# Kernel tuning notes

Measured on AMD Instinct MI355X. Metric: run time of the kernel, lower is better.

## Reference

```python
import jax, jax.numpy as jnp
import numpy as np

ALPHA = 0.2        # LeakyReLU slope
N_NODES = 50000
N_REL = 500


def l2norm(x):
    n = jnp.linalg.norm(x, axis=1, keepdims=True)
    return x / jnp.maximum(n, 1e-12)


def gat_layer(x, edge, eemb, a, a2, concat):
    # x: [N, F]; edge: [2, E] (edge[0]=target, edge[1]=source); eemb: [E, R]
    dst = edge[0]
    h = jnp.concatenate([x[dst], x[edge[1]], eemb], axis=1)          # [E, 2F+R]
    m = h @ a.T                                                       # [E, out]
    p = -jax.nn.leaky_relu(m @ a2[0], ALPHA)                          # [E]
    e = jnp.exp(p)
    rowsum = jax.ops.segment_sum(e, dst, num_segments=N_NODES)       # [N]
    rowsum = jnp.where(rowsum == 0.0, 1e-12, rowsum)
    hp = jax.ops.segment_sum(e[:, None] * m, dst, num_segments=N_NODES) / rowsum[:, None]
    return jax.nn.elu(hp) if concat else hp


def setup_inputs() -> dict:
    key = jax.random.key(0)
    ks = jax.random.split(key, 12)
    E, ENH = 150000, 30000
    D, NHID, H = 200, 100, 2
    return {
        "entity_embeddings": jax.random.normal(ks[0], (N_NODES, D), jnp.float32),
        "relation_embeddings": jax.random.normal(ks[1], (N_REL, D), jnp.float32),
        "W_entities": jax.random.normal(ks[2], (D, NHID * H), jnp.float32) * 0.1,
        "W_gat": jax.random.normal(ks[3], (D, NHID * H), jnp.float32) * 0.1,
        "a_heads": jax.random.normal(ks[4], (H, NHID, 2 * D + D), jnp.float32) * 0.1,
        "a2_heads": jax.random.normal(ks[5], (H, 1, NHID), jnp.float32) * 0.1,
        "a_out": jax.random.normal(ks[6], (NHID * H, 3 * NHID * H), jnp.float32) * 0.1,
        "a2_out": jax.random.normal(ks[7], (1, NHID * H), jnp.float32) * 0.1,
        "batch_entities": jax.random.randint(ks[8], (20000,), 0, N_NODES),
        "edge_list": jax.random.randint(ks[9], (2, E), 0, N_NODES),
        "edge_type": jax.random.randint(ks[10], (E,), 0, N_REL),
        "train_indices_nhop": jax.random.randint(ks[11], (ENH, 4), 0, N_REL),
    }


def reference(entity_embeddings, relation_embeddings, W_entities, W_gat,
              a_heads, a2_heads, a_out, a2_out,
              batch_entities, edge_list, edge_type, train_indices_nhop):
    x = l2norm(entity_embeddings)
    # n-hop edges: (target, source) = (col 3, col 0); relation pair = (col 1, col 2)
    edge_nhop = jnp.stack([train_indices_nhop[:, 3], train_indices_nhop[:, 0]])
    edge_all = jnp.concatenate([edge_list, edge_nhop], axis=1)       # [2, E+Enh]
    eemb1 = jnp.concatenate([
        relation_embeddings[edge_type],
        relation_embeddings[train_indices_nhop[:, 1]] + relation_embeddings[train_indices_nhop[:, 2]],
    ], axis=0)
    # multi-head sparse attention (concat=True -> elu inside)
    heads = jax.vmap(lambda a, a2: gat_layer(x, edge_all, eemb1, a, a2, True))(a_heads, a2_heads)
    x1 = jnp.transpose(heads, (1, 0, 2)).reshape(x.shape[0], -1)     # [N, H*nhid]
    out_rel = relation_embeddings @ W_gat                             # [R, H*nhid]
    eemb2 = jnp.concatenate([
        out_rel[edge_type],
        out_rel[train_indices_nhop[:, 1]] + out_rel[train_indices_nhop[:, 2]],
    ], axis=0)
    out_ent = jax.nn.elu(gat_layer(x1, edge_all, eemb2, a_out, a2_out, False))
    mask = jnp.zeros((x.shape[0],), x.dtype).at[batch_entities].set(1.0)
    out_ent = l2norm(x @ W_entities + mask[:, None] * out_ent)
    return out_ent, out_rel, mask
```

## Files before the change

kernel.cpp:

```cpp
#include <hip/hip_runtime.h>
#include <hip/hip_bf16.h>
#include <math.h>

#define DD   200
#define NHID 100
#define OD   200
#define KP   224
#define PBS  224
#define LDSW 40

typedef __attribute__((ext_vector_type(8))) short short8;
typedef __attribute__((ext_vector_type(4))) float f32x4;

static inline int cdiv(int a, int b) { return (a + b - 1) / b; }

__device__ inline float toF(float x) { return x; }
__device__ inline float toF(__hip_bfloat16 x) { return __bfloat162float(x); }
__device__ inline void storeC(float v, float* p) { *p = v; }
__device__ inline void storeC(float v, __hip_bfloat16* p) { *p = __float2bfloat16(v); }
__device__ inline short bf16s(float f) {
    __hip_bfloat16 h = __float2bfloat16(f);
    short s; __builtin_memcpy(&s, &h, 2); return s;
}

__global__ __launch_bounds__(256)
void rownorm_inv_k(const float* __restrict__ in, float* __restrict__ sc, int M, int Dd)
{
    int wave = (blockIdx.x * blockDim.x + threadIdx.x) >> 6;
    int lane = threadIdx.x & 63;
    if (wave >= M) return;
    float ss = 0.f;
    for (int k = lane; k < Dd; k += 64) {
        float x = in[(size_t)wave * Dd + k];
        ss += x * x;
    }
    for (int o = 32; o > 0; o >>= 1) ss += __shfl_down(ss, o);
    if (lane == 0) sc[wave] = 1.f / fmaxf(sqrtf(ss), 1e-12f);
}

__global__ void prep_bt_l1(const float* __restrict__ ah, __hip_bfloat16* __restrict__ Bt)
{
    int c = blockIdx.x, k = threadIdx.x;
    if (k >= KP) return;
    int seg = c / 100, idx = c - seg * 100;
    int h = seg & 1, off = (seg >> 1) * 200;
    float v = (k < 200) ? ah[(size_t)(h * 100 + idx) * 600 + off + k] : 0.f;
    Bt[(size_t)c * KP + k] = __float2bfloat16(v);
}
__global__ void prep_bt_l2(const float* __restrict__ ao, __hip_bfloat16* __restrict__ Bt)
{
    int c = blockIdx.x, k = threadIdx.x;
    if (k >= KP) return;
    int row = (c < 200) ? c : c - 200;
    int off = (c < 200) ? 0 : 200;
    float v = (k < 200) ? ao[(size_t)row * 600 + off + k] : 0.f;
    Bt[(size_t)c * KP + k] = __float2bfloat16(v);
}
__global__ void prep_bt_fin(const float* __restrict__ W, __hip_bfloat16* __restrict__ Bt)
{
    int c = blockIdx.x, k = threadIdx.x;
    if (k >= KP) return;
    float v = (c < 200 && k < 200) ? W[(size_t)k * 200 + c] : 0.f;
    Bt[(size_t)c * KP + k] = __float2bfloat16(v);
}

__global__ __launch_bounds__(256)
void l1_both_k(const float* __restrict__ ent, const float* __restrict__ nscale,
               const __hip_bfloat16* __restrict__ Bt,
               const float* __restrict__ a2h,
               __hip_bfloat16* __restrict__ x1,
               __hip_bfloat16* __restrict__ pB,
               float* __restrict__ s1,
               int M)
{
    __shared__ __align__(16) __hip_bfloat16 Bs[400 * LDSW];
    int tid = threadIdx.x, wave = tid >> 6, lane = tid & 63;
    int quad = lane >> 4, l16 = lane & 15;
    int m0 = blockIdx.x * 64;
    int arow = m0 + wave * 16 + l16;
    bool rok = arow < M;
    float nsc = rok ? nscale[arow] : 0.f;
    const float* arp = ent + (size_t)arow * DD;

    f32x4 acc[25];
#pragma unroll
    for (int t = 0; t < 25; t++) acc[t] = (f32x4){0.f, 0.f, 0.f, 0.f};

    short8 stg[7];
#pragma unroll
    for (int i = 0; i < 7; i++) {
        int idx = tid + i * 256;
        if (idx < 1600) {
            int r = idx >> 2, c8 = idx & 3;
            stg[i] = *(const short8*)(Bt + (size_t)r * KP + c8 * 8);
        }
    }

    for (int ch = 0; ch < 7; ch++) {
#pragma unroll
        for (int i = 0; i < 7; i++) {
            int idx = tid + i * 256;
            if (idx < 1600) {
                int r = idx >> 2, c8 = idx & 3;
                *(short8*)(Bs + r * LDSW + c8 * 8) = stg[i];
            }
        }
        __syncthreads();
        if (ch < 6) {
            int kb2 = (ch + 1) * 32;
#pragma unroll
            for (int i = 0; i < 7; i++) {
                int idx = tid + i * 256;
                if (idx < 1600) {
                    int r = idx >> 2, c8 = idx & 3;
                    stg[i] = *(const short8*)(Bt + (size_t)r * KP + kb2 + c8 * 8);
                }
            }
        }
        int kb = ch * 32 + quad * 8;
        float av[8];
        if (rok && kb + 8 <= DD) {
            const float4* p = (const float4*)(arp + kb);
            float4 u0 = p[0], u1 = p[1];
            av[0] = u0.x; av[1] = u0.y; av[2] = u0.z; av[3] = u0.w;
            av[4] = u1.x; av[5] = u1.y; av[6] = u1.z; av[7] = u1.w;
        } else {
#pragma unroll
            for (int j = 0; j < 8; j++) av[j] = (rok && kb + j < DD) ? arp[kb + j] : 0.f;
        }
        short8 a;
#pragma unroll
        for (int j = 0; j < 8; j++) a[j] = bf16s(av[j] * nsc);
        const __hip_bfloat16* bp = Bs + (size_t)l16 * LDSW + quad * 8;
#pragma unroll
        for (int t = 0; t < 25; t++) {
            short8 b = *(const short8*)(bp + (size_t)t * 16 * LDSW);
            acc[t] = __builtin_amdgcn_mfma_f32_16x16x32_bf16(a, b, acc[t], 0, 0, 0);
        }
        __syncthreads();
    }

    int orow = m0 + wave * 16 + quad * 4;
    float d0[4] = {0,0,0,0}, d1[4] = {0,0,0,0}, d2[4] = {0,0,0,0}, d3[4] = {0,0,0,0};
#pragma unroll
    for (int t = 0; t < 25; t++) {
        int c = t * 16 + l16;
        int seg = c / 100, idx = c - seg * 100;
        float w = a2h[(seg & 1) * 100 + idx];
#pragma unroll
        for (int i = 0; i < 4; i++) {
            float v = acc[t][i];
            float vw = v * w;
            if (seg == 0) d0[i] += vw;
            else if (seg == 1) d1[i] += vw;
            else if (seg == 2) d2[i] += vw;
            else d3[i] += vw;
            int gm = orow + i;
            if (gm < M) {
                if (seg < 2) x1[(size_t)gm * KP + c] = __float2bfloat16(v);
                else pB[(size_t)gm * PBS + (seg - 2) * 100 + idx] = __float2bfloat16(v);
            }
        }
    }
#pragma unroll
    for (int msk = 1; msk < 16; msk <<= 1)
#pragma unroll
        for (int i = 0; i < 4; i++) {
            d0[i] += __shfl_xor(d0[i], msk);
            d1[i] += __shfl_xor(d1[i], msk);
            d2[i] += __shfl_xor(d2[i], msk);
            d3[i] += __shfl_xor(d3[i], msk);
        }
    if (l16 == 0)
#pragma unroll
        for (int i = 0; i < 4; i++) {
            int gm = orow + i;
            if (gm < M) {
                s1[gm] = d0[i]; s1[M + gm] = d1[i];
                float2 sv; sv.x = d2[i]; sv.y = d3[i];
                *(float2*)((char*)pB + (size_t)gm * (PBS * 2) + 400) = sv;
            }
        }
}

__global__ __launch_bounds__(256)
void l2_proj_k(const __hip_bfloat16* __restrict__ x1,
               const __hip_bfloat16* __restrict__ Bt,
               const float* __restrict__ a2o,
               float* __restrict__ x1A1,
               __hip_bfloat16* __restrict__ x1A2,
               float* __restrict__ s1, int M)
{
    __shared__ __align__(16) __hip_bfloat16 Bs[400 * LDSW];
    int tid = threadIdx.x, wave = tid >> 6, lane = tid & 63;
    int quad = lane >> 4, l16 = lane & 15;
    int m0 = blockIdx.x * 64;
    int arow = m0 + wave * 16 + l16;
    bool rok = arow < M;
    const __hip_bfloat16* arp = x1 + (size_t)arow * KP;

    f32x4 acc[25];
#pragma unroll
    for (int t = 0; t < 25; t++) acc[t] = (f32x4){0.f, 0.f, 0.f, 0.f};

    short8 stg[7];
#pragma unroll
    for (int i = 0; i < 7; i++) {
        int idx = tid + i * 256;
        if (idx < 1600) {
            int r = idx >> 2, c8 = idx & 3;
            stg[i] = *(const short8*)(Bt + (size_t)r * KP + c8 * 8);
        }
    }

    for (int ch = 0; ch < 7; ch++) {
#pragma unroll
        for (int i = 0; i < 7; i++) {
            int idx = tid + i * 256;
            if (idx < 1600) {
                int r = idx >> 2, c8 = idx & 3;
                *(short8*)(Bs + r * LDSW + c8 * 8) = stg[i];
            }
        }
        __syncthreads();
        if (ch < 6) {
            int kb2 = (ch + 1) * 32;
#pragma unroll
            for (int i = 0; i < 7; i++) {
                int idx = tid + i * 256;
                if (idx < 1600) {
                    int r = idx >> 2, c8 = idx & 3;
                    stg[i] = *(const short8*)(Bt + (size_t)r * KP + kb2 + c8 * 8);
                }
            }
        }
        int kb = ch * 32 + quad * 8;
        short8 a = (short8){0,0,0,0,0,0,0,0};
        if (rok) a = *(const short8*)(arp + kb);
        const __hip_bfloat16* bp = Bs + (size_t)l16 * LDSW + quad * 8;
#pragma unroll
        for (int t = 0; t < 25; t++) {
            short8 b = *(const short8*)(bp + (size_t)t * 16 * LDSW);
            acc[t] = __builtin_amdgcn_mfma_f32_16x16x32_bf16(a, b, acc[t], 0, 0, 0);
        }
        __syncthreads();
    }

    int orow = m0 + wave * 16 + quad * 4;
    float dA[4] = {0,0,0,0}, dB[4] = {0,0,0,0};
#pragma unroll
    for (int t = 0; t < 25; t++) {
        int c = t * 16 + l16;
        bool first = c < 200;
        int cc = first ? c : c - 200;
        float w = a2o[cc];
#pragma unroll
        for (int i = 0; i < 4; i++) {
            float v = acc[t][i];
            int gm = orow + i;
            if (first) {
                dA[i] += v * w;
                if (gm < M) x1A1[(size_t)gm * OD + c] = v;
            } else {
                dB[i] += v * w;
                if (gm < M) x1A2[(size_t)gm * PBS + cc] = __float2bfloat16(v);
            }
        }
    }
#pragma unroll
    for (int msk = 1; msk < 16; msk <<= 1)
#pragma unroll
        for (int i = 0; i < 4; i++) {
            dA[i] += __shfl_xor(dA[i], msk);
            dB[i] += __shfl_xor(dB[i], msk);
        }
    if (l16 == 0)
#pragma unroll
        for (int i = 0; i < 4; i++) {
            int gm = orow + i;
            if (gm < M) {
                s1[gm] = dA[i];
                *(float*)((char*)x1A2 + (size_t)gm * (PBS * 2) + 400) = dB[i];
            }
        }
}

__global__ __launch_bounds__(256)
void final_mfma_k(const float* __restrict__ ent, const float* __restrict__ nscale,
                  const __hip_bfloat16* __restrict__ Bt,
                  float* __restrict__ outent, int M)
{
    __shared__ __align__(16) __hip_bfloat16 Bs[208 * LDSW];
    int tid = threadIdx.x, wave = tid >> 6, lane = tid & 63;
    int quad = lane >> 4, l16 = lane & 15;
    int m0 = blockIdx.x * 64;
    int arow = m0 + wave * 16 + l16;
    bool rok = arow < M;
    float nsc = rok ? nscale[arow] : 0.f;
    const float* arp = ent + (size_t)arow * DD;

    f32x4 acc[13];
#pragma unroll
    for (int t = 0; t < 13; t++) acc[t] = (f32x4){0.f, 0.f, 0.f, 0.f};

    short8 stg[4];
#pragma unroll
    for (int i = 0; i < 4; i++) {
        int idx = tid + i * 256;
        if (idx < 832) {
            int r = idx >> 2, c8 = idx & 3;
            stg[i] = *(const short8*)(Bt + (size_t)r * KP + c8 * 8);
        }
    }

    for (int ch = 0; ch < 7; ch++) {
#pragma unroll
        for (int i = 0; i < 4; i++) {
            int idx = tid + i * 256;
            if (idx < 832) {
                int r = idx >> 2, c8 = idx & 3;
                *(short8*)(Bs + r * LDSW + c8 * 8) = stg[i];
            }
        }
        __syncthreads();
        if (ch < 6) {
            int kb2 = (ch + 1) * 32;
#pragma unroll
            for (int i = 0; i < 4; i++) {
                int idx = tid + i * 256;
                if (idx < 832) {
                    int r = idx >> 2, c8 = idx & 3;
                    stg[i] = *(const short8*)(Bt + (size_t)r * KP + kb2 + c8 * 8);
                }
            }
        }
        int kb = ch * 32 + quad * 8;
        float av[8];
        if (rok && kb + 8 <= DD) {
            const float4* p = (const float4*)(arp + kb);
            float4 u0 = p[0], u1 = p[1];
            av[0] = u0.x; av[1] = u0.y; av[2] = u0.z; av[3] = u0.w;
            av[4] = u1.x; av[5] = u1.y; av[6] = u1.z; av[7] = u1.w;
        } else {
#pragma unroll
            for (int j = 0; j < 8; j++) av[j] = (rok && kb + j < DD) ? arp[kb + j] : 0.f;
        }
        short8 a;
#pragma unroll
        for (int j = 0; j < 8; j++) a[j] = bf16s(av[j] * nsc);
        const __hip_bfloat16* bp = Bs + (size_t)l16 * LDSW + quad * 8;
#pragma unroll
        for (int t = 0; t < 13; t++) {
            short8 b = *(const short8*)(bp + (size_t)t * 16 * LDSW);
            acc[t] = __builtin_amdgcn_mfma_f32_16x16x32_bf16(a, b, acc[t], 0, 0, 0);
        }
        __syncthreads();
    }

    int orow = m0 + wave * 16 + quad * 4;
    float ss[4] = {0.f, 0.f, 0.f, 0.f};
#pragma unroll
    for (int t = 0; t < 13; t++) {
        int gn = t * 16 + l16;
#pragma unroll
        for (int i = 0; i < 4; i++) {
            int gm = orow + i;
            float v = 0.f;
            if (gn < OD && gm < M) v = acc[t][i] + outent[(size_t)gm * OD + gn];
            acc[t][i] = v;
            ss[i] += v * v;
        }
    }
#pragma unroll
    for (int msk = 1; msk < 16; msk <<= 1)
#pragma unroll
        for (int i = 0; i < 4; i++) ss[i] += __shfl_xor(ss[i], msk);
    float scl[4];
#pragma unroll
    for (int i = 0; i < 4; i++) scl[i] = 1.f / fmaxf(sqrtf(ss[i]), 1e-12f);
#pragma unroll
    for (int t = 0; t < 13; t++) {
        int gn = t * 16 + l16;
        if (gn >= OD) continue;
#pragma unroll
        for (int i = 0; i < 4; i++) {
            int gm = orow + i;
            if (gm < M) outent[(size_t)gm * OD + gn] = acc[t][i] * scl[i];
        }
    }
}

#define KPAD 48
template<bool BTr, typename AT, typename CT>
__global__ __launch_bounds__(256)
void gemm_mfma_k(const AT* __restrict__ A, int lda, const float* __restrict__ ascale,
                 const float* __restrict__ B, int ldb, int colOff,
                 CT* __restrict__ C, int ldc, int M, int Nc, int K)
{
    __shared__ __align__(16) __hip_bfloat16 As[64][KPAD];
    __shared__ __align__(16) __hip_bfloat16 Bs[64][KPAD];
    int tid  = threadIdx.x;
    int wave = tid >> 6, lane = tid & 63;
    int quad = lane >> 4, l16 = lane & 15;
    int n0 = blockIdx.x * 64, m0 = blockIdx.y * 64;
    f32x4 acc[4];
#pragma unroll
    for (int t = 0; t < 4; t++) acc[t] = (f32x4){0.f, 0.f, 0.f, 0.f};

    for (int k0 = 0; k0 < K; k0 += 32) {
        {
            int m = tid >> 2, kc = (tid & 3) * 8;
            int gm = m0 + m;
            float scale = (ascale && gm < M) ? ascale[gm] : 1.f;
#pragma unroll
            for (int j = 0; j < 8; j++) {
                int gk = k0 + kc + j;
                float v = 0.f;
                if (gm < M && gk < K) v = toF(A[(size_t)gm * lda + gk]) * scale;
                As[m][kc + j] = __float2bfloat16(v);
            }
        }
        if (BTr) {
            int n = tid >> 2, kc = (tid & 3) * 8;
            int gn = n0 + n;
#pragma unroll
            for (int j = 0; j < 8; j++) {
                int gk = k0 + kc + j;
                float v = 0.f;
                if (gn < Nc && gk < K) v = B[(size_t)gn * ldb + colOff + gk];
                Bs[n][kc + j] = __float2bfloat16(v);
            }
        } else {
            int n = tid & 63, kq = tid >> 6;
            int gn = n0 + n;
#pragma unroll
            for (int j = 0; j < 8; j++) {
                int gk = k0 + kq * 8 + j;
                float v = 0.f;
                if (gn < Nc && gk < K) v = B[(size_t)gk * ldb + gn];
                Bs[n][kq * 8 + j] = __float2bfloat16(v);
            }
        }
        __syncthreads();
        short8 a = *(const short8*)&As[wave * 16 + l16][quad * 8];
#pragma unroll
        for (int t = 0; t < 4; t++) {
            short8 b = *(const short8*)&Bs[t * 16 + l16][quad * 8];
            acc[t] = __builtin_amdgcn_mfma_f32_16x16x32_bf16(a, b, acc[t], 0, 0, 0);
        }
        __syncthreads();
    }
#pragma unroll
    for (int t = 0; t < 4; t++) {
        int gn = n0 + t * 16 + l16;
        if (gn >= Nc) continue;
#pragma unroll
        for (int i = 0; i < 4; i++) {
            int gm = m0 + wave * 16 + quad * 4 + i;
            if (gm < M) storeC(acc[t][i], &C[(size_t)gm * ldc + gn]);
        }
    }
}

template<typename T>
__global__ __launch_bounds__(256)
void rowdot_k(const T* __restrict__ mat, int ld, int coff,
              const float* __restrict__ vec,
              float* __restrict__ outp, int M, int Dd)
{
    int wave = (blockIdx.x * blockDim.x + threadIdx.x) >> 6;
    int lane = threadIdx.x & 63;
    if (wave >= M) return;
    float s = 0.f;
    for (int k = lane; k < Dd; k += 64)
        s += toF(mat[(size_t)wave * ld + coff + k]) * vec[k];
    for (int o = 32; o > 0; o >>= 1) s += __shfl_down(s, o);
    if (lane == 0) outp[wave] = s;
}

__device__ inline void decode_edge(const int* __restrict__ el, int E,
                                   const int* __restrict__ etype,
                                   const int* __restrict__ tin, int e,
                                   int& dst, int& src, int& r1, int& r2)
{
    if (e < E) { dst = el[e]; src = el[E + e]; r1 = etype[e]; r2 = -1; }
    else {
        int j = e - E;
        dst = tin[j * 4 + 3]; src = tin[j * 4 + 0];
        r1 = tin[j * 4 + 1];  r2 = tin[j * 4 + 2];
    }
}

__global__ void hist_k(const int* __restrict__ el, int E, const int* __restrict__ etype,
                       const int* __restrict__ tin, int Etot, int* __restrict__ cnt)
{
    int e = blockIdx.x * blockDim.x + threadIdx.x;
    if (e >= Etot) return;
    int dst, src, r1, r2; decode_edge(el, E, etype, tin, e, dst, src, r1, r2);
    atomicAdd(&cnt[dst], 1);
}

__global__ __launch_bounds__(1024)
void scan1_k(const int* __restrict__ cnt, int* __restrict__ start,
             int* __restrict__ aux, int n)
{
    __shared__ int tmp[1024];
    int i = blockIdx.x * 1024 + threadIdx.x;
    int v = (i < n) ? cnt[i] : 0;
    tmp[threadIdx.x] = v;
    __syncthreads();
    for (int o = 1; o < 1024; o <<= 1) {
        int t = (threadIdx.x >= (unsigned)o) ? tmp[threadIdx.x - o] : 0;
        __syncthreads();
        tmp[threadIdx.x] += t;
        __syncthreads();
    }
    if (i < n) start[i] = tmp[threadIdx.x] - v;
    if (threadIdx.x == 1023) aux[blockIdx.x] = tmp[1023];
}

__global__ void scan2_k(int* __restrict__ aux, int nb)
{
    if (threadIdx.x == 0 && blockIdx.x == 0) {
        int s = 0;
        for (int i = 0; i < nb; i++) { int v = aux[i]; aux[i] = s; s += v; }
    }
}

__global__ __launch_bounds__(1024)
void scan3_k(int* __restrict__ start, const int* __restrict__ aux, int n, int Etot)
{
    int i = blockIdx.x * 1024 + threadIdx.x;
    if (i < n) start[i] += aux[blockIdx.x];
    if (i == 0) start[n] = Etot;
}

__global__ void fill_k(const int* __restrict__ el, int E, const int* __restrict__ etype,
                       const int* __restrict__ tin, int Etot,
                       const int* __restrict__ start, int* __restrict__ fill,
                       int2* __restrict__ csr)
{
    int e = blockIdx.x * blockDim.x + threadIdx.x;
    if (e >= Etot) return;
    int dst, src, r1, r2; decode_edge(el, E, etype, tin, e, dst, src, r1, r2);
    int p = start[dst] + atomicAdd(&fill[dst], 1);
    unsigned r2s = (r2 >= 0) ? (unsigned)r2 : 0xFFFFu;
    csr[p] = make_int2(src, (int)((r2s << 16) | (unsigned)r1));
}

__global__ __launch_bounds__(256)
void gather_l1_k(const int* __restrict__ start, const int2* __restrict__ csr,
                 const float* __restrict__ s1,
                 const float* __restrict__ srel2, int R_,
                 const __hip_bfloat16* __restrict__ pB,
                 const float* __restrict__ rpf2,
                 __hip_bfloat16* __restrict__ x1, int N)
{
    int n = (blockIdx.x * blockDim.x + threadIdx.x) >> 6;
    int lane = threadIdx.x & 63;
    if (n >= N) return;
    int b0 = start[n], b1 = start[n + 1];
    float s1h0 = s1[n], s1h1 = s1[N + n];
    float rs0 = 0.f, rs1 = 0.f;
    float a00 = 0.f, a01 = 0.f, a10 = 0.f, a11 = 0.f;
    int k0 = lane, k1 = lane + 64;
    bool k1ok = k1 < 100;
    const float* rph1 = rpf2 + (size_t)R_ * 100;

    int idx = b0;
    for (; idx + 1 < b1; idx += 2) {
        int2 eA = csr[idx], eB = csr[idx + 1];
        unsigned eyA = (unsigned)eA.y, eyB = (unsigned)eB.y;
        int r1A = (int)(eyA & 0xFFFFu), r1B = (int)(eyB & 0xFFFFu);
        unsigned r2A = eyA >> 16, r2B = eyB >> 16;
        const __hip_bfloat16* rA = pB + (size_t)eA.x * PBS;
        const __hip_bfloat16* rB = pB + (size_t)eB.x * PBS;
        float2 sA = *(const float2*)(rA + 200);
        float2 sB = *(const float2*)(rB + 200);
        float vA00 = toF(rA[k0]), vA10 = toF(rA[100 + k0]);
        float vB00 = toF(rB[k0]), vB10 = toF(rB[100 + k0]);
        float vA01 = 0.f, vA11 = 0.f, vB01 = 0.f, vB11 = 0.f;
        if (k1ok) {
            vA01 = toF(rA[k1]); vA11 = toF(rA[100 + k1]);
            vB01 = toF(rB[k1]); vB11 = toF(rB[100 + k1]);
        }
        const float* qA0 = rpf2 + (size_t)r1A * 100;
        const float* qA1 = rph1 + (size_t)r1A * 100;
        const float* qB0 = rpf2 + (size_t)r1B * 100;
        const float* qB1 = rph1 + (size_t)r1B * 100;
        float srA0 = srel2[r1A], srA1 = srel2[R_ + r1A];
        float srB0 = srel2[r1B], srB1 = srel2[R_ + r1B];
        vA00 += qA0[k0]; vA10 += qA1[k0];
        vB00 += qB0[k0]; vB10 += qB1[k0];
        if (k1ok) {
            vA01 += qA0[k1]; vA11 += qA1[k1];
            vB01 += qB0[k1]; vB11 += qB1[k1];
        }
        if (r2A != 0xFFFFu) {
            const float* t0 = rpf2 + (size_t)r2A * 100;
            const float* t1 = rph1 + (size_t)r2A * 100;
            srA0 += srel2[(int)r2A]; srA1 += srel2[R_ + (int)r2A];
            vA00 += t0[k0]; vA10 += t1[k0];
            if (k1ok) { vA01 += t0[k1]; vA11 += t1[k1]; }
        }
        if (r2B != 0xFFFFu) {
            const float* t0 = rpf2 + (size_t)r2B * 100;
            const float* t1 = rph1 + (size_t)r2B * 100;
            srB0 += srel2[(int)r2B]; srB1 += srel2[R_ + (int)r2B];
            vB00 += t0[k0]; vB10 += t1[k0];
            if (k1ok) { vB01 += t0[k1]; vB11 += t1[k1]; }
        }
        float zA0 = s1h0 + sA.x + srA0, zA1 = s1h1 + sA.y + srA1;
        float zB0 = s1h0 + sB.x + srB0, zB1 = s1h1 + sB.y + srB1;
        float wA0 = expf(-(zA0 > 0.f ? zA0 : 0.2f * zA0));
        float wA1 = expf(-(zA1 > 0.f ? zA1 : 0.2f * zA1));
        float wB0 = expf(-(zB0 > 0.f ? zB0 : 0.2f * zB0));
        float wB1 = expf(-(zB1 > 0.f ? zB1 : 0.2f * zB1));
        rs0 += wA0 + wB0; rs1 += wA1 + wB1;
        a00 += wA0 * vA00 + wB0 * vB00;
        a01 += wA0 * vA01 + wB0 * vB01;
        a10 += wA1 * vA10 + wB1 * vB10;
        a11 += wA1 * vA11 + wB1 * vB11;
    }
    if (idx < b1) {
        int2 eg = csr[idx];
        unsigned ey = (unsigned)eg.y;
        int r1 = (int)(ey & 0xFFFFu);
        unsigned r2 = ey >> 16;
        const __hip_bfloat16* rA = pB + (size_t)eg.x * PBS;
        float2 sA = *(const float2*)(rA + 200);
        float v00 = toF(rA[k0]), v10 = toF(rA[100 + k0]);
        float v01 = 0.f, v11 = 0.f;
        if (k1ok) { v01 = toF(rA[k1]); v11 = toF(rA[100 + k1]); }
        const float* q0 = rpf2 + (size_t)r1 * 100;
        const float* q1 = rph1 + (size_t)r1 * 100;
        float sr0 = srel2[r1], sr1 = srel2[R_ + r1];
        v00 += q0[k0]; v10 += q1[k0];
        if (k1ok) { v01 += q0[k1]; v11 += q1[k1]; }
        if (r2 != 0xFFFFu) {
            const float* t0 = rpf2 + (size_t)r2 * 100;
            const float* t1 = rph1 + (size_t)r2 * 100;
            sr0 += srel2[(int)r2]; sr1 += srel2[R_ + (int)r2];
            v00 += t0[k0]; v10 += t1[k0];
            if (k1ok) { v01 += t0[k1]; v11 += t1[k1]; }
        }
        float z0 = s1h0 + sA.x + sr0, z1 = s1h1 + sA.y + sr1;
        float w0 = expf(-(z0 > 0.f ? z0 : 0.2f * z0));
        float w1 = expf(-(z1 > 0.f ? z1 : 0.2f * z1));
        rs0 += w0; rs1 += w1;
        a00 += w0 * v00; a01 += w0 * v01;
        a10 += w1 * v10; a11 += w1 * v11;
    }

    float i0 = rs0 > 0.f ? 1.f / rs0 : 0.f;
    float i1 = rs1 > 0.f ? 1.f / rs1 : 0.f;
    __hip_bfloat16* xr = x1 + (size_t)n * KP;
    float hp;
    hp = rs0 > 0.f ? toF(xr[k0]) + a00 * i0 : 0.f;
    xr[k0] = __float2bfloat16(hp > 0.f ? hp : expf(hp) - 1.f);
    hp = rs1 > 0.f ? toF(xr[100 + k0]) + a10 * i1 : 0.f;
    xr[100 + k0] = __float2bfloat16(hp > 0.f ? hp : expf(hp) - 1.f);
    if (k1ok) {
        hp = rs0 > 0.f ? toF(xr[k1]) + a01 * i0 : 0.f;
        xr[k1] = __float2bfloat16(hp > 0.f ? hp : expf(hp) - 1.f);
        hp = rs1 > 0.f ? toF(xr[100 + k1]) + a11 * i1 : 0.f;
        xr[100 + k1] = __float2bfloat16(hp > 0.f ? hp : expf(hp) - 1.f);
    }
}

__global__ __launch_bounds__(256)
void gather_l2_k(const int* __restrict__ start, const int2* __restrict__ csr,
                 const float* __restrict__ s1,
                 const float* __restrict__ srel,
                 const __hip_bfloat16* __restrict__ x1A2,
                 const float* __restrict__ rpf,
                 const float* __restrict__ maskf,
                 float* __restrict__ outent, int N)
{
    int n = (blockIdx.x * blockDim.x + threadIdx.x) >> 6;
    int lane = threadIdx.x & 63;
    if (n >= N) return;
    int b0 = start[n], b1 = start[n + 1];
    float s1n = s1[n];
    float rs = 0.f;
    float a[4] = {0.f, 0.f, 0.f, 0.f};

    int idx = b0;
    for (; idx + 1 < b1; idx += 2) {
        int2 eA = csr[idx], eB = csr[idx + 1];
        unsigned eyA = (unsigned)eA.y, eyB = (unsigned)eB.y;
        int r1A = (int)(eyA & 0xFFFFu), r1B = (int)(eyB & 0xFFFFu);
        unsigned r2A = eyA >> 16, r2B = eyB >> 16;
        const __hip_bfloat16* xA = x1A2 + (size_t)eA.x * PBS;
        const __hip_bfloat16* xB = x1A2 + (size_t)eB.x * PBS;
        float s2A = *(const float*)(xA + 200);
        float s2B = *(const float*)(xB + 200);
        float srA = srel[r1A] + (r2A != 0xFFFFu ? srel[(int)r2A] : 0.f);
        float srB = srel[r1B] + (r2B != 0xFFFFu ? srel[(int)r2B] : 0.f);
        const float* qA1 = rpf + (size_t)r1A * 200;
        const float* qB1 = rpf + (size_t)r1B * 200;
        const float* qA2 = (r2A != 0xFFFFu) ? (rpf + (size_t)r2A * 200) : nullptr;
        const float* qB2 = (r2B != 0xFFFFu) ? (rpf + (size_t)r2B * 200) : nullptr;
        float zA = s1n + s2A + srA, zB = s1n + s2B + srB;
        float wA = expf(-(zA > 0.f ? zA : 0.2f * zA));
        float wB = expf(-(zB > 0.f ? zB : 0.2f * zB));
        rs += wA + wB;
#pragma unroll
        for (int s = 0; s < 4; s++) {
            int k = lane + 64 * s;
            if (k < 200) {
                float vA = toF(xA[k]) + qA1[k] + (qA2 ? qA2[k] : 0.f);
                float vB = toF(xB[k]) + qB1[k] + (qB2 ? qB2[k] : 0.f);
                a[s] += wA * vA + wB * vB;
            }
        }
    }
    if (idx < b1) {
        int2 eg = csr[idx];
        unsigned ey = (unsigned)eg.y;
        int r1 = (int)(ey & 0xFFFFu);
        unsigned r2 = ey >> 16;
        const __hip_bfloat16* xs = x1A2 + (size_t)eg.x * PBS;
        float s2v = *(const float*)(xs + 200);
        float sr = srel[r1] + (r2 != 0xFFFFu ? srel[(int)r2] : 0.f);
        float z = s1n + s2v + sr;
        float w = expf(-(z > 0.f ? z : 0.2f * z));
        rs += w;
        const float* q1 = rpf + (size_t)r1 * 200;
        const float* q2 = (r2 != 0xFFFFu) ? (rpf + (size_t)r2 * 200) : nullptr;
#pragma unroll
        for (int s = 0; s < 4; s++) {
            int k = lane + 64 * s;
            if (k < 200) {
                float v = toF(xs[k]) + q1[k] + (q2 ? q2[k] : 0.f);
                a[s] += w * v;
            }
        }
    }

    float inv = rs > 0.f ? 1.f / rs : 0.f;
    float mk = maskf[n];
    float* orow = outent + (size_t)n * 200;
#pragma unroll
    for (int s = 0; s < 4; s++) {
        int k = lane + 64 * s;
        if (k < 200) {
            float hp = rs > 0.f ? orow[k] + a[s] * inv : 0.f;
            float e = hp > 0.f ? hp : expf(hp) - 1.f;
            orow[k] = mk * e;
        }
    }
}

__global__ void scatter_mask_k(const int* __restrict__ batch, int NB,
                               float* __restrict__ masko)
{
    int i = blockIdx.x * blockDim.x + threadIdx.x;
    if (i >= NB) return;
    masko[batch[i]] = 1.0f;
}

extern "C" void kernel_launch(void* const* d_in, const int* in_sizes, int n_in,
                              void* d_out, int out_size, void* d_ws, size_t ws_size,
                              hipStream_t stream)
{
    const float* ent      = (const float*)d_in[0];
    const float* rel      = (const float*)d_in[1];
    const float* W_ent    = (const float*)d_in[2];
    const float* W_gat    = (const float*)d_in[3];
    const float* a_heads  = (const float*)d_in[4];
    const float* a2_heads = (const float*)d_in[5];
    const float* a_out    = (const float*)d_in[6];
    const float* a2_out   = (const float*)d_in[7];
    const int* batch = (const int*)d_in[8];
    const int* el    = (const int*)d_in[9];
    const int* etype = (const int*)d_in[10];
    const int* tin   = (const int*)d_in[11];

    const int N   = in_sizes[0] / DD;
    const int R   = in_sizes[1] / DD;
    const int NB  = in_sizes[8];
    const int E   = in_sizes[9] / 2;
    const int ENH = in_sizes[11] / 4;
    const int Etot = E + ENH;

    char* ws = (char*)d_ws;
    size_t off = 0;
    auto take = [&](size_t bytes) { size_t o = off; off += (bytes + 255) & ~(size_t)255; return o; };
    size_t o_R1   = take((size_t)N * KP * 2);
    size_t o_R2   = take((size_t)N * PBS * 2);
    size_t o_rpf  = take((size_t)2 * R * 100 * 4);
    size_t o_bt1  = take((size_t)400 * KP * 2);
    size_t o_bt2  = take((size_t)400 * KP * 2);
    size_t o_btf  = take((size_t)208 * KP * 2);
    size_t o_nsc  = take((size_t)N * 4);
    size_t o_s1   = take((size_t)2 * N * 4);
    size_t o_srel = take((size_t)2 * R * 4);
    size_t o_csr  = take((size_t)Etot * 8);
    size_t o_str  = take((size_t)(N + 1) * 4);
    size_t o_aux  = take((size_t)64 * 4);

    __hip_bfloat16* x1   = (__hip_bfloat16*)(ws + o_R1);
    __hip_bfloat16* pB   = (__hip_bfloat16*)(ws + o_R2);
    __hip_bfloat16* x1A2 = (__hip_bfloat16*)(ws + o_R2);
    float* rpf2   = (float*)(ws + o_rpf);
    __hip_bfloat16* bt1 = (__hip_bfloat16*)(ws + o_bt1);
    __hip_bfloat16* bt2 = (__hip_bfloat16*)(ws + o_bt2);
    __hip_bfloat16* btf = (__hip_bfloat16*)(ws + o_btf);
    float* nscale = (float*)(ws + o_nsc);
    float* s1     = (float*)(ws + o_s1);
    float* srel2  = (float*)(ws + o_srel);
    int2*  csr    = (int2*)(ws + o_csr);
    int*   cnt    = (int*)(ws + o_s1);
    int*   startA = (int*)(ws + o_str);
    int*   aux    = (int*)(ws + o_aux);

    float* out       = (float*)d_out;
    float* out_ent   = out;
    float* out_rel_o = out + (size_t)N * OD;
    float* out_mask  = out + (size_t)N * OD + (size_t)R * OD;

    const int nblk = cdiv(N, 64);
    const int nbScan = cdiv(N, 1024);

    rownorm_inv_k<<<cdiv(N, 4), 256, 0, stream>>>(ent, nscale, N, DD);
    prep_bt_l1<<<400, 256, 0, stream>>>(a_heads, bt1);
    prep_bt_l2<<<400, 256, 0, stream>>>(a_out, bt2);
    prep_bt_fin<<<208, 256, 0, stream>>>(W_ent, btf);
    hipMemsetAsync(x1, 0, (size_t)N * KP * 2, stream);
    gemm_mfma_k<false, float, float><<<dim3(cdiv(OD, 64), cdiv(R, 64)), 256, 0, stream>>>(
        rel, DD, nullptr, W_gat, OD, 0, out_rel_o, OD, R, OD, DD);

    hipMemsetAsync(cnt, 0, (size_t)N * 4, stream);
    hist_k<<<cdiv(Etot, 256), 256, 0, stream>>>(el, E, etype, tin, Etot, cnt);
    scan1_k<<<nbScan, 1024, 0, stream>>>(cnt, startA, aux, N);
    scan2_k<<<1, 64, 0, stream>>>(aux, nbScan);
    scan3_k<<<nbScan, 1024, 0, stream>>>(startA, aux, N, Etot);
    hipMemsetAsync(cnt, 0, (size_t)N * 4, stream);
    fill_k<<<cdiv(Etot, 256), 256, 0, stream>>>(el, E, etype, tin, Etot, startA, cnt, csr);

    l1_both_k<<<nblk, 256, 0, stream>>>(ent, nscale, bt1, a2_heads, x1, pB, s1, N);
    for (int h = 0; h < 2; h++) {
        const float* ah  = a_heads + (size_t)h * NHID * 600;
        const float* a2h = a2_heads + (size_t)h * NHID;
        gemm_mfma_k<true, float, float><<<dim3(cdiv(NHID, 64), cdiv(R, 64)), 256, 0, stream>>>(
            rel, DD, nullptr, ah, 600, 400, rpf2 + (size_t)h * R * NHID, NHID, R, NHID, DD);
        rowdot_k<float><<<cdiv(R, 4), 256, 0, stream>>>(
            rpf2 + (size_t)h * R * NHID, NHID, 0, a2h, srel2 + (size_t)h * R, R, NHID);
    }
    gather_l1_k<<<cdiv(N, 4), 256, 0, stream>>>(
        startA, csr, s1, srel2, R, pB, rpf2, x1, N);

    l2_proj_k<<<nblk, 256, 0, stream>>>(x1, bt2, a2_out, out_ent, x1A2, s1, N);
    gemm_mfma_k<true, float, float><<<dim3(cdiv(OD, 64), cdiv(R, 64)), 256, 0, stream>>>(
        out_rel_o, OD, nullptr, a_out, 600, 400, rpf2, OD, R, OD, OD);
    rowdot_k<float><<<cdiv(R, 4), 256, 0, stream>>>(rpf2, OD, 0, a2_out, srel2, R, OD);

    hipMemsetAsync(out_mask, 0, (size_t)N * 4, stream);
    scatter_mask_k<<<cdiv(NB, 256), 256, 0, stream>>>(batch, NB, out_mask);
    gather_l2_k<<<cdiv(N, 4), 256, 0, stream>>>(
        startA, csr, s1, srel2, x1A2, rpf2, out_mask, out_ent, N);

    final_mfma_k<<<nblk, 256, 0, stream>>>(ent, nscale, btf, out_ent, N);
}
```

Measured before the change: 521.3 us.

## Interleave head data and unroll edge gathers by four with packed loads

The per-source projection buffer pB and the relation projection/score buffers now store the two heads interleaved, so gather_l1 reads both heads with a single 32-bit or float2 load. Both gather kernels are rewritten to process four edges per iteration without branches, masking invalid edges and absent second relations with zero weights. The layer-2 gather also uses paired bf16/float2 loads and stores. This is meant to raise memory-level parallelism and cut load instruction count in the latency-bound CSR gathers, at the cost of more registers and some wasted loads on padded edges.

```diff
diff --git a/kernel.cpp b/kernel.cpp
--- a/kernel.cpp
+++ b/kernel.cpp
@@ -22,6 +22,8 @@
     __hip_bfloat16 h = __float2bfloat16(f);
     short s; __builtin_memcpy(&s, &h, 2); return s;
 }
+__device__ inline float bfLo(unsigned u) { return __uint_as_float(u << 16); }
+__device__ inline float bfHi(unsigned u) { return __uint_as_float(u & 0xFFFF0000u); }
 
 __global__ __launch_bounds__(256)
 void rownorm_inv_k(const float* __restrict__ in, float* __restrict__ sc, int M, int Dd)
@@ -158,7 +160,7 @@
             int gm = orow + i;
             if (gm < M) {
                 if (seg < 2) x1[(size_t)gm * KP + c] = __float2bfloat16(v);
-                else pB[(size_t)gm * PBS + (seg - 2) * 100 + idx] = __float2bfloat16(v);
+                else pB[(size_t)gm * PBS + idx * 2 + (seg - 2)] = __float2bfloat16(v);
             }
         }
     }
@@ -395,7 +397,8 @@
 __global__ __launch_bounds__(256)
 void gemm_mfma_k(const AT* __restrict__ A, int lda, const float* __restrict__ ascale,
                  const float* __restrict__ B, int ldb, int colOff,
-                 CT* __restrict__ C, int ldc, int M, int Nc, int K)
+                 CT* __restrict__ C, int ldc, int cs, int co,
+                 int M, int Nc, int K)
 {
     __shared__ __align__(16) __hip_bfloat16 As[64][KPAD];
     __shared__ __align__(16) __hip_bfloat16 Bs[64][KPAD];
@@ -457,25 +460,25 @@
 #pragma unroll
         for (int i = 0; i < 4; i++) {
             int gm = m0 + wave * 16 + quad * 4 + i;
-            if (gm < M) storeC(acc[t][i], &C[(size_t)gm * ldc + gn]);
+            if (gm < M) storeC(acc[t][i], &C[(size_t)gm * ldc + (size_t)gn * cs + co]);
         }
     }
 }
 
 template<typename T>
 __global__ __launch_bounds__(256)
-void rowdot_k(const T* __restrict__ mat, int ld, int coff,
+void rowdot_k(const T* __restrict__ mat, int ld, int coff, int ks,
               const float* __restrict__ vec,
-              float* __restrict__ outp, int M, int Dd)
+              float* __restrict__ outp, int os, int oo, int M, int Dd)
 {
     int wave = (blockIdx.x * blockDim.x + threadIdx.x) >> 6;
     int lane = threadIdx.x & 63;
     if (wave >= M) return;
     float s = 0.f;
     for (int k = lane; k < Dd; k += 64)
-        s += toF(mat[(size_t)wave * ld + coff + k]) * vec[k];
+        s += toF(mat[(size_t)wave * ld + coff + (size_t)k * ks]) * vec[k];
     for (int o = 32; o > 0; o >>= 1) s += __shfl_down(s, o);
-    if (lane == 0) outp[wave] = s;
+    if (lane == 0) outp[wave * os + oo] = s;
 }
 
 __device__ inline void decode_edge(const int* __restrict__ el, int E,
@@ -551,7 +554,7 @@
 __global__ __launch_bounds__(256)
 void gather_l1_k(const int* __restrict__ start, const int2* __restrict__ csr,
                  const float* __restrict__ s1,
-                 const float* __restrict__ srel2, int R_,
+                 const float* __restrict__ srel2,
                  const __hip_bfloat16* __restrict__ pB,
                  const float* __restrict__ rpf2,
                  __hip_bfloat16* __restrict__ x1, int N)
@@ -562,108 +565,67 @@
     int b0 = start[n], b1 = start[n + 1];
     float s1h0 = s1[n], s1h1 = s1[N + n];
     float rs0 = 0.f, rs1 = 0.f;
-    float a00 = 0.f, a01 = 0.f, a10 = 0.f, a11 = 0.f;
+    float2 acc0 = {0.f, 0.f};
+    float2 acc1 = {0.f, 0.f};
     int k0 = lane, k1 = lane + 64;
     bool k1ok = k1 < 100;
-    const float* rph1 = rpf2 + (size_t)R_ * 100;
-
-    int idx = b0;
-    for (; idx + 1 < b1; idx += 2) {
-        int2 eA = csr[idx], eB = csr[idx + 1];
-        unsigned eyA = (unsigned)eA.y, eyB = (unsigned)eB.y;
-        int r1A = (int)(eyA & 0xFFFFu), r1B = (int)(eyB & 0xFFFFu);
-        unsigned r2A = eyA >> 16, r2B = eyB >> 16;
-        const __hip_bfloat16* rA = pB + (size_t)eA.x * PBS;
-        const __hip_bfloat16* rB = pB + (size_t)eB.x * PBS;
-        float2 sA = *(const float2*)(rA + 200);
-        float2 sB = *(const float2*)(rB + 200);
-        float vA00 = toF(rA[k0]), vA10 = toF(rA[100 + k0]);
-        float vB00 = toF(rB[k0]), vB10 = toF(rB[100 + k0]);
-        float vA01 = 0.f, vA11 = 0.f, vB01 = 0.f, vB11 = 0.f;
-        if (k1ok) {
-            vA01 = toF(rA[k1]); vA11 = toF(rA[100 + k1]);
-            vB01 = toF(rB[k1]); vB11 = toF(rB[100 + k1]);
-        }
-        const float* qA0 = rpf2 + (size_t)r1A * 100;
-        const float* qA1 = rph1 + (size_t)r1A * 100;
-        const float* qB0 = rpf2 + (size_t)r1B * 100;
-        const float* qB1 = rph1 + (size_t)r1B * 100;
-        float srA0 = srel2[r1A], srA1 = srel2[R_ + r1A];
-        float srB0 = srel2[r1B], srB1 = srel2[R_ + r1B];
-        vA00 += qA0[k0]; vA10 += qA1[k0];
-        vB00 += qB0[k0]; vB10 += qB1[k0];
-        if (k1ok) {
-            vA01 += qA0[k1]; vA11 += qA1[k1];
-            vB01 += qB0[k1]; vB11 += qB1[k1];
-        }
-        if (r2A != 0xFFFFu) {
-            const float* t0 = rpf2 + (size_t)r2A * 100;
-            const float* t1 = rph1 + (size_t)r2A * 100;
-            srA0 += srel2[(int)r2A]; srA1 += srel2[R_ + (int)r2A];
-            vA00 += t0[k0]; vA10 += t1[k0];
-            if (k1ok) { vA01 += t0[k1]; vA11 += t1[k1]; }
-        }
-        if (r2B != 0xFFFFu) {
-            const float* t0 = rpf2 + (size_t)r2B * 100;
-            const float* t1 = rph1 + (size_t)r2B * 100;
-            srB0 += srel2[(int)r2B]; srB1 += srel2[R_ + (int)r2B];
-            vB00 += t0[k0]; vB10 += t1[k0];
-            if (k1ok) { vB01 += t0[k1]; vB11 += t1[k1]; }
-        }
-        float zA0 = s1h0 + sA.x + srA0, zA1 = s1h1 + sA.y + srA1;
-        float zB0 = s1h0 + sB.x + srB0, zB1 = s1h1 + sB.y + srB1;
-        float wA0 = expf(-(zA0 > 0.f ? zA0 : 0.2f * zA0));
-        float wA1 = expf(-(zA1 > 0.f ? zA1 : 0.2f * zA1));
-        float wB0 = expf(-(zB0 > 0.f ? zB0 : 0.2f * zB0));
-        float wB1 = expf(-(zB1 > 0.f ? zB1 : 0.2f * zB1));
-        rs0 += wA0 + wB0; rs1 += wA1 + wB1;
-        a00 += wA0 * vA00 + wB0 * vB00;
-        a01 += wA0 * vA01 + wB0 * vB01;
-        a10 += wA1 * vA10 + wB1 * vB10;
-        a11 += wA1 * vA11 + wB1 * vB11;
-    }
-    if (idx < b1) {
-        int2 eg = csr[idx];
-        unsigned ey = (unsigned)eg.y;
-        int r1 = (int)(ey & 0xFFFFu);
-        unsigned r2 = ey >> 16;
-        const __hip_bfloat16* rA = pB + (size_t)eg.x * PBS;
-        float2 sA = *(const float2*)(rA + 200);
-        float v00 = toF(rA[k0]), v10 = toF(rA[100 + k0]);
-        float v01 = 0.f, v11 = 0.f;
-        if (k1ok) { v01 = toF(rA[k1]); v11 = toF(rA[100 + k1]); }
-        const float* q0 = rpf2 + (size_t)r1 * 100;
-        const float* q1 = rph1 + (size_t)r1 * 100;
-        float sr0 = srel2[r1], sr1 = srel2[R_ + r1];
-        v00 += q0[k0]; v10 += q1[k0];
-        if (k1ok) { v01 += q0[k1]; v11 += q1[k1]; }
-        if (r2 != 0xFFFFu) {
-            const float* t0 = rpf2 + (size_t)r2 * 100;
-            const float* t1 = rph1 + (size_t)r2 * 100;
-            sr0 += srel2[(int)r2]; sr1 += srel2[R_ + (int)r2];
-            v00 += t0[k0]; v10 += t1[k0];
-            if (k1ok) { v01 += t0[k1]; v11 += t1[k1]; }
-        }
-        float z0 = s1h0 + sA.x + sr0, z1 = s1h1 + sA.y + sr1;
-        float w0 = expf(-(z0 > 0.f ? z0 : 0.2f * z0));
-        float w1 = expf(-(z1 > 0.f ? z1 : 0.2f * z1));
-        rs0 += w0; rs1 += w1;
-        a00 += w0 * v00; a01 += w0 * v01;
-        a10 += w1 * v10; a11 += w1 * v11;
+    int k1c = k1ok ? k1 : 0;
+
+    for (int base = b0; base < b1; base += 4) {
+        float2 vk0[4], vk1[4];
+        float w0[4], w1[4];
+#pragma unroll
+        for (int u = 0; u < 4; u++) {
+            int id = base + u;
+            bool val = id < b1;
+            int2 eg = csr[val ? id : b0];
+            unsigned ey = (unsigned)eg.y;
+            int r1 = (int)(ey & 0xFFFFu);
+            unsigned r2u = ey >> 16;
+            bool has2 = (r2u != 0xFFFFu);
+            int r2 = has2 ? (int)r2u : 0;
+            float f2 = has2 ? 1.f : 0.f;
+            const __hip_bfloat16* rA = pB + (unsigned)((unsigned)eg.x * PBS);
+            float2 sA = *(const float2*)(rA + 200);
+            unsigned pw0 = *(const unsigned*)(rA + 2 * k0);
+            unsigned pw1 = *(const unsigned*)(rA + 2 * k1c);
+            const float2* q1 = (const float2*)(rpf2 + (unsigned)r1 * 200);
+            const float2* q2 = (const float2*)(rpf2 + (unsigned)r2 * 200);
+            float2 sr1v = *(const float2*)(srel2 + r1 * 2);
+            float2 sr2v = *(const float2*)(srel2 + r2 * 2);
+            float2 q1a = q1[k0], q1b = q1[k1c];
+            float2 q2a = q2[k0], q2b = q2[k1c];
+            vk0[u].x = bfLo(pw0) + q1a.x + f2 * q2a.x;
+            vk0[u].y = bfHi(pw0) + q1a.y + f2 * q2a.y;
+            vk1[u].x = bfLo(pw1) + q1b.x + f2 * q2b.x;
+            vk1[u].y = bfHi(pw1) + q1b.y + f2 * q2b.y;
+            float z0 = s1h0 + sA.x + sr1v.x + f2 * sr2v.x;
+            float z1 = s1h1 + sA.y + sr1v.y + f2 * sr2v.y;
+            float e0 = expf(-(z0 > 0.f ? z0 : 0.2f * z0));
+            float e1 = expf(-(z1 > 0.f ? z1 : 0.2f * z1));
+            w0[u] = val ? e0 : 0.f;
+            w1[u] = val ? e1 : 0.f;
+        }
+#pragma unroll
+        for (int u = 0; u < 4; u++) {
+            rs0 += w0[u]; rs1 += w1[u];
+            acc0.x += w0[u] * vk0[u].x; acc0.y += w1[u] * vk0[u].y;
+            acc1.x += w0[u] * vk1[u].x; acc1.y += w1[u] * vk1[u].y;
+        }
     }
 
     float i0 = rs0 > 0.f ? 1.f / rs0 : 0.f;
     float i1 = rs1 > 0.f ? 1.f / rs1 : 0.f;
     __hip_bfloat16* xr = x1 + (size_t)n * KP;
     float hp;
-    hp = rs0 > 0.f ? toF(xr[k0]) + a00 * i0 : 0.f;
+    hp = rs0 > 0.f ? toF(xr[k0]) + acc0.x * i0 : 0.f;
     xr[k0] = __float2bfloat16(hp > 0.f ? hp : expf(hp) - 1.f);
-    hp = rs1 > 0.f ? toF(xr[100 + k0]) + a10 * i1 : 0.f;
+    hp = rs1 > 0.f ? toF(xr[100 + k0]) + acc0.y * i1 : 0.f;
     xr[100 + k0] = __float2bfloat16(hp > 0.f ? hp : expf(hp) - 1.f);
     if (k1ok) {
-        hp = rs0 > 0.f ? toF(xr[k1]) + a01 * i0 : 0.f;
+        hp = rs0 > 0.f ? toF(xr[k1]) + acc1.x * i0 : 0.f;
         xr[k1] = __float2bfloat16(hp > 0.f ? hp : expf(hp) - 1.f);
-        hp = rs1 > 0.f ? toF(xr[100 + k1]) + a11 * i1 : 0.f;
+        hp = rs1 > 0.f ? toF(xr[100 + k1]) + acc1.y * i1 : 0.f;
         xr[100 + k1] = __float2bfloat16(hp > 0.f ? hp : expf(hp) - 1.f);
     }
 }
@@ -683,72 +645,73 @@
     int b0 = start[n], b1 = start[n + 1];
     float s1n = s1[n];
     float rs = 0.f;
-    float a[4] = {0.f, 0.f, 0.f, 0.f};
-
-    int idx = b0;
-    for (; idx + 1 < b1; idx += 2) {
-        int2 eA = csr[idx], eB = csr[idx + 1];
-        unsigned eyA = (unsigned)eA.y, eyB = (unsigned)eB.y;
-        int r1A = (int)(eyA & 0xFFFFu), r1B = (int)(eyB & 0xFFFFu);
-        unsigned r2A = eyA >> 16, r2B = eyB >> 16;
-        const __hip_bfloat16* xA = x1A2 + (size_t)eA.x * PBS;
-        const __hip_bfloat16* xB = x1A2 + (size_t)eB.x * PBS;
-        float s2A = *(const float*)(xA + 200);
-        float s2B = *(const float*)(xB + 200);
-        float srA = srel[r1A] + (r2A != 0xFFFFu ? srel[(int)r2A] : 0.f);
-        float srB = srel[r1B] + (r2B != 0xFFFFu ? srel[(int)r2B] : 0.f);
-        const float* qA1 = rpf + (size_t)r1A * 200;
-        const float* qB1 = rpf + (size_t)r1B * 200;
-        const float* qA2 = (r2A != 0xFFFFu) ? (rpf + (size_t)r2A * 200) : nullptr;
-        const float* qB2 = (r2B != 0xFFFFu) ? (rpf + (size_t)r2B * 200) : nullptr;
-        float zA = s1n + s2A + srA, zB = s1n + s2B + srB;
-        float wA = expf(-(zA > 0.f ? zA : 0.2f * zA));
-        float wB = expf(-(zB > 0.f ? zB : 0.2f * zB));
-        rs += wA + wB;
-#pragma unroll
-        for (int s = 0; s < 4; s++) {
-            int k = lane + 64 * s;
-            if (k < 200) {
-                float vA = toF(xA[k]) + qA1[k] + (qA2 ? qA2[k] : 0.f);
-                float vB = toF(xB[k]) + qB1[k] + (qB2 ? qB2[k] : 0.f);
-                a[s] += wA * vA + wB * vB;
-            }
-        }
-    }
-    if (idx < b1) {
-        int2 eg = csr[idx];
-        unsigned ey = (unsigned)eg.y;
-        int r1 = (int)(ey & 0xFFFFu);
-        unsigned r2 = ey >> 16;
-        const __hip_bfloat16* xs = x1A2 + (size_t)eg.x * PBS;
-        float s2v = *(const float*)(xs + 200);
-        float sr = srel[r1] + (r2 != 0xFFFFu ? srel[(int)r2] : 0.f);
-        float z = s1n + s2v + sr;
-        float w = expf(-(z > 0.f ? z : 0.2f * z));
-        rs += w;
-        const float* q1 = rpf + (size_t)r1 * 200;
-        const float* q2 = (r2 != 0xFFFFu) ? (rpf + (size_t)r2 * 200) : nullptr;
-#pragma unroll
-        for (int s = 0; s < 4; s++) {
-            int k = lane + 64 * s;
-            if (k < 200) {
-                float v = toF(xs[k]) + q1[k] + (q2 ? q2[k] : 0.f);
-                a[s] += w * v;
-            }
+    float2 a0 = {0.f, 0.f};
+    float2 a1 = {0.f, 0.f};
+    int j0 = 2 * lane;
+    bool j1ok = lane < 36;
+    int j1 = j1ok ? (128 + 2 * lane) : 0;
+
+    for (int base = b0; base < b1; base += 4) {
+        float2 v0[4], v1[4];
+        float w[4];
+#pragma unroll
+        for (int u = 0; u < 4; u++) {
+            int id = base + u;
+            bool val = id < b1;
+            int2 eg = csr[val ? id : b0];
+            unsigned ey = (unsigned)eg.y;
+            int r1 = (int)(ey & 0xFFFFu);
+            unsigned r2u = ey >> 16;
+            bool has2 = (r2u != 0xFFFFu);
+            int r2 = has2 ? (int)r2u : 0;
+            float f2 = has2 ? 1.f : 0.f;
+            const __hip_bfloat16* xs = x1A2 + (unsigned)((unsigned)eg.x * PBS);
+            float s2v = *(const float*)(xs + 200);
+            unsigned xw0 = *(const unsigned*)(xs + j0);
+            unsigned xw1 = *(const unsigned*)(xs + j1);
+            const float* q1 = rpf + (unsigned)r1 * 200;
+            const float* q2 = rpf + (unsigned)r2 * 200;
+            float2 q1a = *(const float2*)(q1 + j0);
+            float2 q1b = *(const float2*)(q1 + j1);
+            float2 q2a = *(const float2*)(q2 + j0);
+            float2 q2b = *(const float2*)(q2 + j1);
+            float sr = srel[r1] + f2 * srel[r2];
+            v0[u].x = bfLo(xw0) + q1a.x + f2 * q2a.x;
+            v0[u].y = bfHi(xw0) + q1a.y + f2 * q2a.y;
+            v1[u].x = bfLo(xw1) + q1b.x + f2 * q2b.x;
+            v1[u].y = bfHi(xw1) + q1b.y + f2 * q2b.y;
+            float z = s1n + s2v + sr;
+            float e = expf(-(z > 0.f ? z : 0.2f * z));
+            w[u] = val ? e : 0.f;
+        }
+#pragma unroll
+        for (int u = 0; u < 4; u++) {
+            rs += w[u];
+            a0.x += w[u] * v0[u].x; a0.y += w[u] * v0[u].y;
+            a1.x += w[u] * v1[u].x; a1.y += w[u] * v1[u].y;
         }
     }
 
     float inv = rs > 0.f ? 1.f / rs : 0.f;
     float mk = maskf[n];
     float* orow = outent + (size_t)n * 200;
-#pragma unroll
-    for (int s = 0; s < 4; s++) {
-        int k = lane + 64 * s;
-        if (k < 200) {
-            float hp = rs > 0.f ? orow[k] + a[s] * inv : 0.f;
-            float e = hp > 0.f ? hp : expf(hp) - 1.f;
-            orow[k] = mk * e;
-        }
+    {
+        float2 o = *(const float2*)(orow + j0);
+        float hpx = rs > 0.f ? o.x + a0.x * inv : 0.f;
+        float hpy = rs > 0.f ? o.y + a0.y * inv : 0.f;
+        float2 r;
+        r.x = mk * (hpx > 0.f ? hpx : expf(hpx) - 1.f);
+        r.y = mk * (hpy > 0.f ? hpy : expf(hpy) - 1.f);
+        *(float2*)(orow + j0) = r;
+    }
+    if (j1ok) {
+        float2 o = *(const float2*)(orow + j1);
+        float hpx = rs > 0.f ? o.x + a1.x * inv : 0.f;
+        float hpy = rs > 0.f ? o.y + a1.y * inv : 0.f;
+        float2 r;
+        r.x = mk * (hpx > 0.f ? hpx : expf(hpx) - 1.f);
+        r.y = mk * (hpy > 0.f ? hpy : expf(hpy) - 1.f);
+        *(float2*)(orow + j1) = r;
     }
 }
 
@@ -829,7 +792,7 @@
     prep_bt_fin<<<208, 256, 0, stream>>>(W_ent, btf);
     hipMemsetAsync(x1, 0, (size_t)N * KP * 2, stream);
     gemm_mfma_k<false, float, float><<<dim3(cdiv(OD, 64), cdiv(R, 64)), 256, 0, stream>>>(
-        rel, DD, nullptr, W_gat, OD, 0, out_rel_o, OD, R, OD, DD);
+        rel, DD, nullptr, W_gat, OD, 0, out_rel_o, OD, 1, 0, R, OD, DD);
 
     hipMemsetAsync(cnt, 0, (size_t)N * 4, stream);
     hist_k<<<cdiv(Etot, 256), 256, 0, stream>>>(el, E, etype, tin, Etot, cnt);
@@ -844,17 +807,17 @@
         const float* ah  = a_heads + (size_t)h * NHID * 600;
         const float* a2h = a2_heads + (size_t)h * NHID;
         gemm_mfma_k<true, float, float><<<dim3(cdiv(NHID, 64), cdiv(R, 64)), 256, 0, stream>>>(
-            rel, DD, nullptr, ah, 600, 400, rpf2 + (size_t)h * R * NHID, NHID, R, NHID, DD);
+            rel, DD, nullptr, ah, 600, 400, rpf2, 200, 2, h, R, NHID, DD);
         rowdot_k<float><<<cdiv(R, 4), 256, 0, stream>>>(
-            rpf2 + (size_t)h * R * NHID, NHID, 0, a2h, srel2 + (size_t)h * R, R, NHID);
+            rpf2, 200, h, 2, a2h, srel2, 2, h, R, NHID);
     }
     gather_l1_k<<<cdiv(N, 4), 256, 0, stream>>>(
-        startA, csr, s1, srel2, R, pB, rpf2, x1, N);
+        startA, csr, s1, srel2, pB, rpf2, x1, N);
 
     l2_proj_k<<<nblk, 256, 0, stream>>>(x1, bt2, a2_out, out_ent, x1A2, s1, N);
     gemm_mfma_k<true, float, float><<<dim3(cdiv(OD, 64), cdiv(R, 64)), 256, 0, stream>>>(
-        out_rel_o, OD, nullptr, a_out, 600, 400, rpf2, OD, R, OD, OD);
-    rowdot_k<float><<<cdiv(R, 4), 256, 0, stream>>>(rpf2, OD, 0, a2_out, srel2, R, OD);
+        out_rel_o, OD, nullptr, a_out, 600, 400, rpf2, OD, 1, 0, R, OD, OD);
+    rowdot_k<float><<<cdiv(R, 4), 256, 0, stream>>>(rpf2, OD, 0, 1, a2_out, srel2, 1, 0, R, OD);
 
     hipMemsetAsync(out_mask, 0, (size_t)N * 4, stream);
     scatter_mask_k<<<cdiv(NB, 256), 256, 0, stream>>>(batch, NB, out_mask);
```

New measurement: 568.6 us. 1.09x slower.
